# Optimization experiments

Measured on AMD Instinct MI355X. Metric: run time of the kernel, lower is better.

Reference implementation:

```python
import jax, jax.numpy as jnp
import numpy as np

N_HEAD = 4
D_MODEL = 256
D_K = D_MODEL // N_HEAD  # 64


def setup_inputs() -> dict:
    key = jax.random.key(0)
    ks = jax.random.split(key, 7)
    B, S = 4, 2048
    # xavier-uniform-ish scale for weights
    def xav(k, shape):
        fan_in, fan_out = shape[1], shape[0]
        lim = float(np.sqrt(6.0 / (fan_in + fan_out)))
        return jax.random.uniform(k, shape, jnp.float32, -lim, lim)
    return {
        "q": jax.random.normal(ks[0], (B, S, D_MODEL), jnp.float32),
        "k": jax.random.normal(ks[1], (B, S, D_MODEL), jnp.float32),
        "v": jax.random.normal(ks[2], (B, S, D_MODEL), jnp.float32),
        # per-head projection weights, stacked: [H, d_k, d_model]
        "Wq": jnp.stack([xav(jax.random.fold_in(ks[3], i), (D_K, D_MODEL)) for i in range(N_HEAD)]),
        "Wk": jnp.stack([xav(jax.random.fold_in(ks[4], i), (D_K, D_MODEL)) for i in range(N_HEAD)]),
        # v_layer is SHARED across heads: [d_v, d_model]
        "Wv": xav(ks[5], (D_K, D_MODEL)),
        # output projection: [d_model, d_v]
        "Wh": xav(ks[6], (D_MODEL, D_K)),
    }


def reference(q, k, v, Wq, Wk, Wv, Wh):
    # per-head projections (batched over heads)
    qs = jnp.einsum('bsd,hed->bhse', q, Wq)          # [B,H,S,d_k]
    ks_ = jnp.einsum('bsd,hed->bhse', k, Wk)         # [B,H,S,d_k]
    vs = jnp.einsum('bsd,ed->bse', v, Wv)            # shared v: [B,S,d_v]
    scale = jnp.sqrt(jnp.asarray(D_K, jnp.float32))
    scores = jnp.einsum('bhse,bhte->bhst', qs, ks_) / scale  # [B,H,S,S]
    attn = jax.nn.softmax(scores, axis=-1)
    heads = jnp.einsum('bhst,bte->bhse', attn, vs)   # [B,H,S,d_v]
    pooled = jnp.mean(heads, axis=1)                 # mean over heads: [B,S,d_v]
    out = jnp.einsum('bse,fe->bsf', pooled, Wh)      # [B,S,d_model]
    # original stacks attns at dim=2 -> [B,S,H,S]
    attn_out = jnp.transpose(attn, (0, 2, 1, 3))
    return out, attn_out
```

## Files before the change

kernel.cpp:

```cpp
#include <hip/hip_runtime.h>
#include <hip/hip_bf16.h>
#include <math.h>

#define B 4
#define S 2048
#define H 4
#define DK 64
#define DM 256

using bf16x8 = __attribute__((ext_vector_type(8))) short;
using bf16x4 = __attribute__((ext_vector_type(4))) short;
using f32x4 = __attribute__((ext_vector_type(4))) float;
typedef unsigned char u8;

__device__ inline ushort f2b(float f) {
  __hip_bfloat16 h = __float2bfloat16(f);
  ushort u; __builtin_memcpy(&u, &h, 2); return u;
}
__device__ inline float b2f(ushort u) {
  __hip_bfloat16 h; __builtin_memcpy(&h, &u, 2); return __bfloat162float(h);
}
__device__ inline float b2f_s(short s) { return b2f((ushort)s); }
__device__ inline bf16x8 ld8(const ushort* p) {
  return *reinterpret_cast<const bf16x8*>(p);
}
__device__ inline bf16x4 ld4(const ushort* p) {
  return *reinterpret_cast<const bf16x4*>(p);
}
#define MFMA(a, b, c) __builtin_amdgcn_mfma_f32_16x16x32_bf16((a), (b), (c), 0, 0, 0)

#if __has_builtin(__builtin_amdgcn_mfma_f32_16x16x16bf16_1k)
__device__ inline f32x4 MFMA16(bf16x4 a, bf16x4 b, f32x4 c) {
  return __builtin_amdgcn_mfma_f32_16x16x16bf16_1k(a, b, c, 0, 0, 0);
}
#else
__device__ inline f32x4 MFMA16(bf16x4 a, bf16x4 b, f32x4 c) {
  asm("v_mfma_f32_16x16x16_bf16 %0, %1, %2, %0" : "+v"(c) : "v"(a), "v"(b));
  return c;
}
#endif

__global__ __launch_bounds__(256) void wsplit_kernel(
    const float* __restrict__ Wq, const float* __restrict__ Wk,
    const float* __restrict__ Wv, const float* __restrict__ Wh,
    ushort* __restrict__ wqh, ushort* __restrict__ wql,
    ushort* __restrict__ wkh, ushort* __restrict__ wkl,
    ushort* __restrict__ wvh, ushort* __restrict__ wvl,
    ushort* __restrict__ whh, ushort* __restrict__ whl) {
  const int row = blockIdx.x;
  const int t = threadIdx.x;
  if (row < 576) {
    const float* src; ushort* dh; ushort* dl; int r;
    if (row < 256) { src = Wq; dh = wqh; dl = wql; r = row; }
    else if (row < 512) { src = Wk; dh = wkh; dl = wkl; r = row - 256; }
    else { src = Wv; dh = wvh; dl = wvl; r = row - 512; }
    const float v = src[(size_t)r * DM + t];
    const ushort hi = f2b(v);
    dh[(size_t)r * DM + t] = hi;
    dl[(size_t)r * DM + t] = f2b(v - b2f(hi));
  } else if (t < 64) {
    const int r = row - 576;
    const float v = Wh[(size_t)r * DK + t];
    const ushort hi = f2b(v);
    whh[(size_t)r * DK + t] = hi;
    whl[(size_t)r * DK + t] = f2b(v - b2f(hi));
  }
}

__global__ __launch_bounds__(256) void proj_qk2(
    const float* __restrict__ q, const float* __restrict__ k,
    const ushort* __restrict__ wqh, const ushort* __restrict__ wql,
    const ushort* __restrict__ wkh, const ushort* __restrict__ wkl,
    ushort* __restrict__ qhi, ushort* __restrict__ qlo,
    ushort* __restrict__ khi, ushort* __restrict__ klo) {
  const int which = blockIdx.x >> 9;
  const int sub = blockIdx.x & 511;
  const int tile = sub & 127;
  const int h = sub >> 7;
  const float* x = which ? k : q;
  const ushort* wh = which ? wkh : wqh;
  const ushort* wl = which ? wkl : wql;
  ushort* ohi = which ? khi : qhi;
  ushort* olo = which ? klo : qlo;

  const int wid = threadIdx.x >> 6;
  const int lane = threadIdx.x & 63;
  const int l15 = lane & 15, g = lane >> 4;
  const int row0 = tile * 64 + wid * 16;

  bf16x8 ah[8], al[8];
  const float* xrow = x + (size_t)(row0 + l15) * DM;
#pragma unroll
  for (int ks = 0; ks < 8; ++ks) {
    float4 f0 = *(const float4*)(xrow + ks * 32 + 8 * g);
    float4 f1 = *(const float4*)(xrow + ks * 32 + 8 * g + 4);
    float fv[8] = {f0.x, f0.y, f0.z, f0.w, f1.x, f1.y, f1.z, f1.w};
    bf16x8 h8, l8;
#pragma unroll
    for (int j = 0; j < 8; ++j) {
      ushort hu = f2b(fv[j]);
      h8[j] = (short)hu;
      l8[j] = (short)f2b(fv[j] - b2f(hu));
    }
    ah[ks] = h8; al[ks] = l8;
  }

  f32x4 acc[4];
#pragma unroll
  for (int n = 0; n < 4; ++n) acc[n] = (f32x4){0.f, 0.f, 0.f, 0.f};

#pragma unroll
  for (int n = 0; n < 4; ++n) {
    const ushort* wrh = wh + (size_t)(h * DK + n * 16 + l15) * DM + 8 * g;
    const ushort* wrl = wl + (size_t)(h * DK + n * 16 + l15) * DM + 8 * g;
#pragma unroll
    for (int ks = 0; ks < 8; ++ks) {
      bf16x8 bh = ld8(wrh + ks * 32);
      bf16x8 bl = ld8(wrl + ks * 32);
      acc[n] = MFMA(ah[ks], bh, acc[n]);
      acc[n] = MFMA(al[ks], bh, acc[n]);
      acc[n] = MFMA(ah[ks], bl, acc[n]);
    }
  }

#pragma unroll
  for (int n = 0; n < 4; ++n) {
    const int e = n * 16 + l15;
#pragma unroll
    for (int r = 0; r < 4; ++r) {
      const int tok = row0 + 4 * g + r;
      const int b = tok >> 11, s = tok & (S - 1);
      const size_t idx = ((size_t)((b * H + h) * S + s)) * DK + e;
      const float val = acc[n][r];
      const ushort hu = f2b(val);
      ohi[idx] = hu;
      olo[idx] = f2b(val - b2f(hu));
    }
  }
}

__global__ __launch_bounds__(256) void proj_v(
    const float* __restrict__ x, const ushort* __restrict__ wh,
    const ushort* __restrict__ wl, ushort* __restrict__ vT) {
  const int wid = threadIdx.x >> 6;
  const int lane = threadIdx.x & 63;
  const int l15 = lane & 15, g = lane >> 4;
  const int row0 = blockIdx.x * 64 + wid * 16;

  bf16x8 ah[8], al[8];
  const float* xrow = x + (size_t)(row0 + l15) * DM;
#pragma unroll
  for (int ks = 0; ks < 8; ++ks) {
    float4 f0 = *(const float4*)(xrow + ks * 32 + 8 * g);
    float4 f1 = *(const float4*)(xrow + ks * 32 + 8 * g + 4);
    float fv[8] = {f0.x, f0.y, f0.z, f0.w, f1.x, f1.y, f1.z, f1.w};
    bf16x8 h8, l8;
#pragma unroll
    for (int j = 0; j < 8; ++j) {
      ushort hu = f2b(fv[j]);
      h8[j] = (short)hu;
      l8[j] = (short)f2b(fv[j] - b2f(hu));
    }
    ah[ks] = h8; al[ks] = l8;
  }

  f32x4 acc[4];
#pragma unroll
  for (int n = 0; n < 4; ++n) acc[n] = (f32x4){0.f, 0.f, 0.f, 0.f};
#pragma unroll
  for (int n = 0; n < 4; ++n) {
    const ushort* wrh = wh + (size_t)(n * 16 + l15) * DM + 8 * g;
    const ushort* wrl = wl + (size_t)(n * 16 + l15) * DM + 8 * g;
#pragma unroll
    for (int ks = 0; ks < 8; ++ks) {
      bf16x8 bh = ld8(wrh + ks * 32);
      bf16x8 bl = ld8(wrl + ks * 32);
      acc[n] = MFMA(ah[ks], bh, acc[n]);
      acc[n] = MFMA(al[ks], bh, acc[n]);
      acc[n] = MFMA(ah[ks], bl, acc[n]);
    }
  }
#pragma unroll
  for (int n = 0; n < 4; ++n) {
    const int e = n * 16 + l15;
#pragma unroll
    for (int r = 0; r < 4; ++r) {
      const int tok = row0 + 4 * g + r;
      const int b = tok >> 11, s = tok & (S - 1);
      vT[((size_t)b * DK + e) * S + s] = f2b(acc[n][r]);
    }
  }
}

__global__ __launch_bounds__(512) void attn_kernel(
    const ushort* __restrict__ qhi, const ushort* __restrict__ qlo,
    const ushort* __restrict__ khi, const ushort* __restrict__ klo,
    const ushort* __restrict__ vT,
    float* __restrict__ attn_out, float* __restrict__ heads) {
  __shared__ __align__(16) u8 kst[2][8192];
  __shared__ __align__(16) u8 vst[2][5120];

  const int tid = threadIdx.x;
  const int wid = tid >> 6;
  const int lane = tid & 63;
  const int l15 = lane & 15, g = lane >> 4;
  const int bid = blockIdx.x;
  const int swz = (bid & 7) * 32 + (bid >> 3);
  const int qt = swz & 15;
  const int h = (swz >> 4) & 3;
  const int b = swz >> 6;
  const int row0 = qt * 128 + wid * 16;
  const float SC = 0.125f;

  const size_t bh = (size_t)(b * H + h);
  const ushort* qbh = qhi + (bh * S + row0 + l15) * DK;
  const ushort* qbl = qlo + (bh * S + row0 + l15) * DK;
  const bf16x8 aqh0 = ld8(qbh + 8 * g), aqh1 = ld8(qbh + 32 + 8 * g);
  const bf16x8 aql0 = ld8(qbl + 8 * g), aql1 = ld8(qbl + 32 + 8 * g);
  const ushort* kbh = khi + bh * S * DK;
  const ushort* kbl = klo + bh * S * DK;
  const ushort* vTb = vT + (size_t)b * DK * S;

  const int role = tid >> 8;
  const int t8 = tid & 255;
  const int skey = t8 >> 3, sslot = t8 & 7;
  const int sgslot = sslot ^ (skey & 7);
  const ushort* ksrc = role ? kbl : kbh;
  const int kdst = role * 4096 + t8 * 16;
  const int sdim = tid >> 3, sk8 = tid & 7;

  const int fx0 = l15 * 128 + ((g ^ (l15 & 7)) << 4);
  const int fx1 = l15 * 128 + (((4 + g) ^ (l15 & 7)) << 4);
  const int fy0 = fx0 + 2048;
  const int fy1 = fx1 + 2048;

  float ssum = 0.f;
  if (role == 0)
    *(bf16x8*)(&kst[0][t8 * 16]) = ld8(kbh + (size_t)skey * DK + sgslot * 8);
  __syncthreads();
  for (int c = 0; c < 64; ++c) {
    const int p = c & 1;
    bf16x8 rkh;
    if (c + 1 < 64 && role == 0)
      rkh = ld8(kbh + (size_t)((c + 1) * 32 + skey) * DK + sgslot * 8);
    const u8* kb = kst[p];
    bf16x8 bh0 = *(const bf16x8*)(kb + fx0);
    bf16x8 bh1 = *(const bf16x8*)(kb + fx1);
    bf16x8 ch0 = *(const bf16x8*)(kb + fy0);
    bf16x8 ch1 = *(const bf16x8*)(kb + fy1);
    f32x4 a0 = {0.f, 0.f, 0.f, 0.f}, a1 = {0.f, 0.f, 0.f, 0.f};
    a0 = MFMA(bh0, aqh0, a0); a0 = MFMA(bh1, aqh1, a0);
    a1 = MFMA(ch0, aqh0, a1); a1 = MFMA(ch1, aqh1, a1);
    ssum += ((__expf(a0[0] * SC) + __expf(a0[1] * SC)) +
             (__expf(a0[2] * SC) + __expf(a0[3] * SC))) +
            ((__expf(a1[0] * SC) + __expf(a1[1] * SC)) +
             (__expf(a1[2] * SC) + __expf(a1[3] * SC)));
    if (c + 1 < 64 && role == 0) *(bf16x8*)(&kst[p ^ 1][t8 * 16]) = rkh;
    __syncthreads();
  }
  ssum += __shfl_xor(ssum, 16, 64);
  ssum += __shfl_xor(ssum, 32, 64);
  const float inv = 1.f / ssum;

  f32x4 hacc[4] = {{0.f, 0.f, 0.f, 0.f}, {0.f, 0.f, 0.f, 0.f},
                   {0.f, 0.f, 0.f, 0.f}, {0.f, 0.f, 0.f, 0.f}};
  float* arow = attn_out + (((size_t)(b * S + row0 + l15)) * H + h) * S;

  *(bf16x8*)(&kst[0][kdst]) = ld8(ksrc + (size_t)skey * DK + sgslot * 8);
  *(bf16x4*)(&vst[0][sdim * 80 + sk8 * 8]) = ld4(vTb + (size_t)sdim * S + sk8 * 4);
  __syncthreads();

  for (int c = 0; c < 64; ++c) {
    const int p = c & 1;
    const int t0 = c * 32;
    bf16x8 rk; bf16x4 rv;
    if (c + 1 < 64) {
      const size_t t1 = (size_t)(c + 1) * 32;
      rk = ld8(ksrc + (t1 + skey) * DK + sgslot * 8);
      rv = ld4(vTb + (size_t)sdim * S + t1 + sk8 * 4);
    }
    const u8* kb = kst[p];
    const u8* vb = vst[p];
    bf16x8 bh0 = *(const bf16x8*)(kb + fx0);
    bf16x8 bh1 = *(const bf16x8*)(kb + fx1);
    bf16x8 ch0 = *(const bf16x8*)(kb + fy0);
    bf16x8 ch1 = *(const bf16x8*)(kb + fy1);
    bf16x8 bl0 = *(const bf16x8*)(kb + 4096 + fx0);
    bf16x8 bl1 = *(const bf16x8*)(kb + 4096 + fx1);
    bf16x8 cl0 = *(const bf16x8*)(kb + 4096 + fy0);
    bf16x8 cl1 = *(const bf16x8*)(kb + 4096 + fy1);
    f32x4 a0 = {0.f, 0.f, 0.f, 0.f}, a1 = {0.f, 0.f, 0.f, 0.f};
    a0 = MFMA(bh0, aqh0, a0); a0 = MFMA(bh1, aqh1, a0);
    a0 = MFMA(bl0, aqh0, a0); a0 = MFMA(bl1, aqh1, a0);
    a0 = MFMA(bh0, aql0, a0); a0 = MFMA(bh1, aql1, a0);
    a1 = MFMA(ch0, aqh0, a1); a1 = MFMA(ch1, aqh1, a1);
    a1 = MFMA(cl0, aqh0, a1); a1 = MFMA(cl1, aqh1, a1);
    a1 = MFMA(ch0, aql0, a1); a1 = MFMA(ch1, aql1, a1);

    const float p0 = __expf(a0[0] * SC) * inv;
    const float p1 = __expf(a0[1] * SC) * inv;
    const float p2 = __expf(a0[2] * SC) * inv;
    const float p3 = __expf(a0[3] * SC) * inv;
    const float p4 = __expf(a1[0] * SC) * inv;
    const float p5 = __expf(a1[1] * SC) * inv;
    const float p6 = __expf(a1[2] * SC) * inv;
    const float p7 = __expf(a1[3] * SC) * inv;

    f32x4 o0 = {p0, p1, p2, p3};
    f32x4 o1 = {p4, p5, p6, p7};
    __builtin_nontemporal_store(o0, (f32x4*)(arow + t0 + 4 * g));
    __builtin_nontemporal_store(o1, (f32x4*)(arow + t0 + 16 + 4 * g));

    bf16x4 pa0, pa1;
    pa0[0] = (short)f2b(p0); pa0[1] = (short)f2b(p1);
    pa0[2] = (short)f2b(p2); pa0[3] = (short)f2b(p3);
    pa1[0] = (short)f2b(p4); pa1[1] = (short)f2b(p5);
    pa1[2] = (short)f2b(p6); pa1[3] = (short)f2b(p7);

#pragma unroll
    for (int n = 0; n < 4; ++n) {
      bf16x4 vb0 = *(const bf16x4*)(vb + (n * 16 + l15) * 80 + 8 * g);
      bf16x4 vb1 = *(const bf16x4*)(vb + (n * 16 + l15) * 80 + 32 + 8 * g);
      hacc[n] = MFMA16(pa0, vb0, hacc[n]);
      hacc[n] = MFMA16(pa1, vb1, hacc[n]);
    }

    if (c + 1 < 64) {
      *(bf16x8*)(&kst[p ^ 1][kdst]) = rk;
      *(bf16x4*)(&vst[p ^ 1][sdim * 80 + sk8 * 8]) = rv;
    }
    __syncthreads();
  }

#pragma unroll
  for (int n = 0; n < 4; ++n)
#pragma unroll
    for (int r = 0; r < 4; ++r)
      heads[(bh * S + row0 + 4 * g + r) * DK + n * 16 + l15] = hacc[n][r];
}

__global__ __launch_bounds__(256) void out_mfma(
    const float* __restrict__ heads, const ushort* __restrict__ whh,
    const ushort* __restrict__ whl, float* __restrict__ out) {
  const int wid = threadIdx.x >> 6;
  const int lane = threadIdx.x & 63;
  const int l15 = lane & 15, g = lane >> 4;
  const int row0 = blockIdx.x * 16;
  const int tok = row0 + l15;
  const int b = tok >> 11, s = tok & (S - 1);

  bf16x8 ah[2], al[2];
  const float* hp0 = heads + ((size_t)((b * H + 0) * S + s)) * DK;
  const size_t hstride = (size_t)S * DK;
#pragma unroll
  for (int c = 0; c < 2; ++c) {
    const int d0 = c * 32 + 8 * g;
    float4 s0 = {0.f, 0.f, 0.f, 0.f}, s1 = {0.f, 0.f, 0.f, 0.f};
#pragma unroll
    for (int hh = 0; hh < H; ++hh) {
      const float* hp = hp0 + hh * hstride + d0;
      float4 x0 = *(const float4*)hp;
      float4 x1 = *(const float4*)(hp + 4);
      s0.x += x0.x; s0.y += x0.y; s0.z += x0.z; s0.w += x0.w;
      s1.x += x1.x; s1.y += x1.y; s1.z += x1.z; s1.w += x1.w;
    }
    float fv[8] = {s0.x * 0.25f, s0.y * 0.25f, s0.z * 0.25f, s0.w * 0.25f,
                   s1.x * 0.25f, s1.y * 0.25f, s1.z * 0.25f, s1.w * 0.25f};
    bf16x8 h8, l8;
#pragma unroll
    for (int j = 0; j < 8; ++j) {
      ushort hu = f2b(fv[j]);
      h8[j] = (short)hu;
      l8[j] = (short)f2b(fv[j] - b2f(hu));
    }
    ah[c] = h8; al[c] = l8;
  }

  f32x4 acc[4];
#pragma unroll
  for (int n = 0; n < 4; ++n) acc[n] = (f32x4){0.f, 0.f, 0.f, 0.f};
#pragma unroll
  for (int n = 0; n < 4; ++n) {
    const int f = wid * 64 + n * 16 + l15;
    const ushort* brh = whh + (size_t)f * DK + 8 * g;
    const ushort* brl = whl + (size_t)f * DK + 8 * g;
#pragma unroll
    for (int c = 0; c < 2; ++c) {
      bf16x8 bh = ld8(brh + c * 32);
      bf16x8 bl = ld8(brl + c * 32);
      acc[n] = MFMA(ah[c], bh, acc[n]);
      acc[n] = MFMA(al[c], bh, acc[n]);
      acc[n] = MFMA(ah[c], bl, acc[n]);
    }
  }

#pragma unroll
  for (int n = 0; n < 4; ++n) {
    const int f = wid * 64 + n * 16 + l15;
#pragma unroll
    for (int r = 0; r < 4; ++r)
      out[(size_t)(row0 + 4 * g + r) * DM + f] = acc[n][r];
  }
}

extern "C" void kernel_launch(void* const* d_in, const int* in_sizes, int n_in,
                              void* d_out, int out_size, void* d_ws, size_t ws_size,
                              hipStream_t stream) {
  const float* q = (const float*)d_in[0];
  const float* k = (const float*)d_in[1];
  const float* v = (const float*)d_in[2];
  const float* Wq = (const float*)d_in[3];
  const float* Wk = (const float*)d_in[4];
  const float* Wv = (const float*)d_in[5];
  const float* Wh = (const float*)d_in[6];

  float* out = (float*)d_out;
  float* attn_out = out + (size_t)B * S * DM;

  const size_t n1 = (size_t)B * H * S * DK;
  ushort* qhi = (ushort*)d_ws;
  ushort* qlo = qhi + n1;
  ushort* khi = qlo + n1;
  ushort* klo = khi + n1;
  ushort* vT = klo + n1;
  float* heads = (float*)(vT + (size_t)B * DK * S);
  ushort* wqh = (ushort*)(heads + n1);
  ushort* wql = wqh + (size_t)H * DK * DM;
  ushort* wkh = wql + (size_t)H * DK * DM;
  ushort* wkl = wkh + (size_t)H * DK * DM;
  ushort* wvh = wkl + (size_t)H * DK * DM;
  ushort* wvl = wvh + (size_t)DK * DM;
  ushort* whh = wvl + (size_t)DK * DM;
  ushort* whl = whh + (size_t)DM * DK;

  wsplit_kernel<<<832, 256, 0, stream>>>(Wq, Wk, Wv, Wh, wqh, wql, wkh, wkl,
                                         wvh, wvl, whh, whl);
  proj_qk2<<<1024, 256, 0, stream>>>(q, k, wqh, wql, wkh, wkl, qhi, qlo, khi, klo);
  proj_v<<<128, 256, 0, stream>>>(v, wvh, wvl, vT);
  attn_kernel<<<256, 512, 0, stream>>>(qhi, qlo, khi, klo, vT, attn_out, heads);
  out_mfma<<<512, 256, 0, stream>>>(heads, whh, whl, out);
}
```

Baseline: 170.4 us.

## Merge Q/K/V projections into one launch and enlarge attention key tiles

The V projection is folded into the Q/K projection kernel as extra blocks, which removes one kernel launch and lets V share the same wave. In the attention kernel the key chunk grows from 32 to 128 keys in the row-sum pass and to 64 keys in the output pass, with all 512 threads now loading K hi and lo. This cuts the number of loop iterations and barriers. MFMA sections are wrapped in s_setprio, at the cost of doubled LDS use, which may reduce occupancy.

New measurement: 183.1 us. +7.4%, slower.

```diff
diff --git a/kernel.cpp b/kernel.cpp
--- a/kernel.cpp
+++ b/kernel.cpp
@@ -20,12 +20,8 @@
 __device__ inline float b2f(ushort u) {
   __hip_bfloat16 h; __builtin_memcpy(&h, &u, 2); return __bfloat162float(h);
 }
-__device__ inline float b2f_s(short s) { return b2f((ushort)s); }
 __device__ inline bf16x8 ld8(const ushort* p) {
   return *reinterpret_cast<const bf16x8*>(p);
-}
-__device__ inline bf16x4 ld4(const ushort* p) {
-  return *reinterpret_cast<const bf16x4*>(p);
 }
 #define MFMA(a, b, c) __builtin_amdgcn_mfma_f32_16x16x32_bf16((a), (b), (c), 0, 0, 0)
 
@@ -67,26 +63,35 @@
   }
 }
 
-__global__ __launch_bounds__(256) void proj_qk2(
+__global__ __launch_bounds__(256) void proj_all(
     const float* __restrict__ q, const float* __restrict__ k,
+    const float* __restrict__ v,
     const ushort* __restrict__ wqh, const ushort* __restrict__ wql,
     const ushort* __restrict__ wkh, const ushort* __restrict__ wkl,
+    const ushort* __restrict__ wvh, const ushort* __restrict__ wvl,
     ushort* __restrict__ qhi, ushort* __restrict__ qlo,
-    ushort* __restrict__ khi, ushort* __restrict__ klo) {
-  const int which = blockIdx.x >> 9;
-  const int sub = blockIdx.x & 511;
-  const int tile = sub & 127;
-  const int h = sub >> 7;
-  const float* x = which ? k : q;
-  const ushort* wh = which ? wkh : wqh;
-  const ushort* wl = which ? wkl : wql;
-  ushort* ohi = which ? khi : qhi;
-  ushort* olo = which ? klo : qlo;
-
+    ushort* __restrict__ khi, ushort* __restrict__ klo,
+    ushort* __restrict__ vT) {
+  const int bid = blockIdx.x;
   const int wid = threadIdx.x >> 6;
   const int lane = threadIdx.x & 63;
   const int l15 = lane & 15, g = lane >> 4;
-  const int row0 = tile * 64 + wid * 16;
+
+  const float* x; const ushort* wh; const ushort* wl;
+  int row0, h;
+  if (bid < 1024) {
+    const int which = bid >> 9;
+    const int sub = bid & 511;
+    const int tile = sub & 127;
+    h = sub >> 7;
+    x = which ? k : q;
+    wh = which ? wkh : wqh;
+    wl = which ? wkl : wql;
+    row0 = tile * 64 + wid * 16;
+  } else {
+    x = v; wh = wvh; wl = wvl; h = 0;
+    row0 = (bid - 1024) * 64 + wid * 16;
+  }
 
   bf16x8 ah[8], al[8];
   const float* xrow = x + (size_t)(row0 + l15) * DM;
@@ -108,7 +113,6 @@
   f32x4 acc[4];
 #pragma unroll
   for (int n = 0; n < 4; ++n) acc[n] = (f32x4){0.f, 0.f, 0.f, 0.f};
-
 #pragma unroll
   for (int n = 0; n < 4; ++n) {
     const ushort* wrh = wh + (size_t)(h * DK + n * 16 + l15) * DM + 8 * g;
@@ -123,71 +127,33 @@
     }
   }
 
-#pragma unroll
-  for (int n = 0; n < 4; ++n) {
-    const int e = n * 16 + l15;
-#pragma unroll
-    for (int r = 0; r < 4; ++r) {
-      const int tok = row0 + 4 * g + r;
-      const int b = tok >> 11, s = tok & (S - 1);
-      const size_t idx = ((size_t)((b * H + h) * S + s)) * DK + e;
-      const float val = acc[n][r];
-      const ushort hu = f2b(val);
-      ohi[idx] = hu;
-      olo[idx] = f2b(val - b2f(hu));
-    }
-  }
-}
-
-__global__ __launch_bounds__(256) void proj_v(
-    const float* __restrict__ x, const ushort* __restrict__ wh,
-    const ushort* __restrict__ wl, ushort* __restrict__ vT) {
-  const int wid = threadIdx.x >> 6;
-  const int lane = threadIdx.x & 63;
-  const int l15 = lane & 15, g = lane >> 4;
-  const int row0 = blockIdx.x * 64 + wid * 16;
-
-  bf16x8 ah[8], al[8];
-  const float* xrow = x + (size_t)(row0 + l15) * DM;
-#pragma unroll
-  for (int ks = 0; ks < 8; ++ks) {
-    float4 f0 = *(const float4*)(xrow + ks * 32 + 8 * g);
-    float4 f1 = *(const float4*)(xrow + ks * 32 + 8 * g + 4);
-    float fv[8] = {f0.x, f0.y, f0.z, f0.w, f1.x, f1.y, f1.z, f1.w};
-    bf16x8 h8, l8;
-#pragma unroll
-    for (int j = 0; j < 8; ++j) {
-      ushort hu = f2b(fv[j]);
-      h8[j] = (short)hu;
-      l8[j] = (short)f2b(fv[j] - b2f(hu));
-    }
-    ah[ks] = h8; al[ks] = l8;
-  }
-
-  f32x4 acc[4];
-#pragma unroll
-  for (int n = 0; n < 4; ++n) acc[n] = (f32x4){0.f, 0.f, 0.f, 0.f};
-#pragma unroll
-  for (int n = 0; n < 4; ++n) {
-    const ushort* wrh = wh + (size_t)(n * 16 + l15) * DM + 8 * g;
-    const ushort* wrl = wl + (size_t)(n * 16 + l15) * DM + 8 * g;
-#pragma unroll
-    for (int ks = 0; ks < 8; ++ks) {
-      bf16x8 bh = ld8(wrh + ks * 32);
-      bf16x8 bl = ld8(wrl + ks * 32);
-      acc[n] = MFMA(ah[ks], bh, acc[n]);
-      acc[n] = MFMA(al[ks], bh, acc[n]);
-      acc[n] = MFMA(ah[ks], bl, acc[n]);
-    }
-  }
-#pragma unroll
-  for (int n = 0; n < 4; ++n) {
-    const int e = n * 16 + l15;
-#pragma unroll
-    for (int r = 0; r < 4; ++r) {
-      const int tok = row0 + 4 * g + r;
-      const int b = tok >> 11, s = tok & (S - 1);
-      vT[((size_t)b * DK + e) * S + s] = f2b(acc[n][r]);
+  if (bid < 1024) {
+    ushort* ohi = (bid >> 9) ? khi : qhi;
+    ushort* olo = (bid >> 9) ? klo : qlo;
+#pragma unroll
+    for (int n = 0; n < 4; ++n) {
+      const int e = n * 16 + l15;
+#pragma unroll
+      for (int r = 0; r < 4; ++r) {
+        const int tok = row0 + 4 * g + r;
+        const int b = tok >> 11, s = tok & (S - 1);
+        const size_t idx = ((size_t)((b * H + h) * S + s)) * DK + e;
+        const float val = acc[n][r];
+        const ushort hu = f2b(val);
+        ohi[idx] = hu;
+        olo[idx] = f2b(val - b2f(hu));
+      }
+    }
+  } else {
+#pragma unroll
+    for (int n = 0; n < 4; ++n) {
+      const int e = n * 16 + l15;
+#pragma unroll
+      for (int r = 0; r < 4; ++r) {
+        const int tok = row0 + 4 * g + r;
+        const int b = tok >> 11, s = tok & (S - 1);
+        vT[((size_t)b * DK + e) * S + s] = f2b(acc[n][r]);
+      }
     }
   }
 }
@@ -197,8 +163,8 @@
     const ushort* __restrict__ khi, const ushort* __restrict__ klo,
     const ushort* __restrict__ vT,
     float* __restrict__ attn_out, float* __restrict__ heads) {
-  __shared__ __align__(16) u8 kst[2][8192];
-  __shared__ __align__(16) u8 vst[2][5120];
+  __shared__ __align__(16) u8 kst[2][16384];
+  __shared__ __align__(16) u8 vst[2][10240];
 
   const int tid = threadIdx.x;
   const int wid = tid >> 6;
@@ -221,42 +187,45 @@
   const ushort* kbl = klo + bh * S * DK;
   const ushort* vTb = vT + (size_t)b * DK * S;
 
-  const int role = tid >> 8;
-  const int t8 = tid & 255;
-  const int skey = t8 >> 3, sslot = t8 & 7;
+  const int skey = tid >> 3, sslot = tid & 7;
   const int sgslot = sslot ^ (skey & 7);
-  const ushort* ksrc = role ? kbl : kbh;
-  const int kdst = role * 4096 + t8 * 16;
   const int sdim = tid >> 3, sk8 = tid & 7;
 
   const int fx0 = l15 * 128 + ((g ^ (l15 & 7)) << 4);
   const int fx1 = l15 * 128 + (((4 + g) ^ (l15 & 7)) << 4);
-  const int fy0 = fx0 + 2048;
-  const int fy1 = fx1 + 2048;
 
   float ssum = 0.f;
-  if (role == 0)
-    *(bf16x8*)(&kst[0][t8 * 16]) = ld8(kbh + (size_t)skey * DK + sgslot * 8);
-  __syncthreads();
-  for (int c = 0; c < 64; ++c) {
-    const int p = c & 1;
-    bf16x8 rkh;
-    if (c + 1 < 64 && role == 0)
-      rkh = ld8(kbh + (size_t)((c + 1) * 32 + skey) * DK + sgslot * 8);
-    const u8* kb = kst[p];
-    bf16x8 bh0 = *(const bf16x8*)(kb + fx0);
-    bf16x8 bh1 = *(const bf16x8*)(kb + fx1);
-    bf16x8 ch0 = *(const bf16x8*)(kb + fy0);
-    bf16x8 ch1 = *(const bf16x8*)(kb + fy1);
-    f32x4 a0 = {0.f, 0.f, 0.f, 0.f}, a1 = {0.f, 0.f, 0.f, 0.f};
-    a0 = MFMA(bh0, aqh0, a0); a0 = MFMA(bh1, aqh1, a0);
-    a1 = MFMA(ch0, aqh0, a1); a1 = MFMA(ch1, aqh1, a1);
-    ssum += ((__expf(a0[0] * SC) + __expf(a0[1] * SC)) +
-             (__expf(a0[2] * SC) + __expf(a0[3] * SC))) +
-            ((__expf(a1[0] * SC) + __expf(a1[1] * SC)) +
-             (__expf(a1[2] * SC) + __expf(a1[3] * SC)));
-    if (c + 1 < 64 && role == 0) *(bf16x8*)(&kst[p ^ 1][t8 * 16]) = rkh;
+  {
+    *(bf16x8*)(&kst[0][tid * 16]) = ld8(kbh + (size_t)skey * DK + sgslot * 8);
+    *(bf16x8*)(&kst[0][8192 + tid * 16]) =
+        ld8(kbh + (size_t)(skey + 64) * DK + sgslot * 8);
     __syncthreads();
+    for (int c = 0; c < 16; ++c) {
+      const int p = c & 1;
+      bf16x8 r0, r1;
+      if (c + 1 < 16) {
+        const size_t t1 = (size_t)(c + 1) * 128;
+        r0 = ld8(kbh + (t1 + skey) * DK + sgslot * 8);
+        r1 = ld8(kbh + (t1 + skey + 64) * DK + sgslot * 8);
+      }
+      const u8* kb = kst[p];
+      __builtin_amdgcn_s_setprio(1);
+#pragma unroll
+      for (int kg = 0; kg < 8; ++kg) {
+        bf16x8 bh0 = *(const bf16x8*)(kb + kg * 2048 + fx0);
+        bf16x8 bh1 = *(const bf16x8*)(kb + kg * 2048 + fx1);
+        f32x4 a = {0.f, 0.f, 0.f, 0.f};
+        a = MFMA(bh0, aqh0, a); a = MFMA(bh1, aqh1, a);
+        ssum += (__expf(a[0] * SC) + __expf(a[1] * SC)) +
+                (__expf(a[2] * SC) + __expf(a[3] * SC));
+      }
+      __builtin_amdgcn_s_setprio(0);
+      if (c + 1 < 16) {
+        *(bf16x8*)(&kst[p ^ 1][tid * 16]) = r0;
+        *(bf16x8*)(&kst[p ^ 1][8192 + tid * 16]) = r1;
+      }
+      __syncthreads();
+    }
   }
   ssum += __shfl_xor(ssum, 16, 64);
   ssum += __shfl_xor(ssum, 32, 64);
@@ -266,68 +235,57 @@
                    {0.f, 0.f, 0.f, 0.f}, {0.f, 0.f, 0.f, 0.f}};
   float* arow = attn_out + (((size_t)(b * S + row0 + l15)) * H + h) * S;
 
-  *(bf16x8*)(&kst[0][kdst]) = ld8(ksrc + (size_t)skey * DK + sgslot * 8);
-  *(bf16x4*)(&vst[0][sdim * 80 + sk8 * 8]) = ld4(vTb + (size_t)sdim * S + sk8 * 4);
+  *(bf16x8*)(&kst[0][tid * 16]) = ld8(kbh + (size_t)skey * DK + sgslot * 8);
+  *(bf16x8*)(&kst[0][8192 + tid * 16]) = ld8(kbl + (size_t)skey * DK + sgslot * 8);
+  *(bf16x8*)(&vst[0][sdim * 160 + sk8 * 16]) = ld8(vTb + (size_t)sdim * S + sk8 * 8);
   __syncthreads();
 
-  for (int c = 0; c < 64; ++c) {
+  for (int c = 0; c < 32; ++c) {
     const int p = c & 1;
-    const int t0 = c * 32;
-    bf16x8 rk; bf16x4 rv;
-    if (c + 1 < 64) {
-      const size_t t1 = (size_t)(c + 1) * 32;
-      rk = ld8(ksrc + (t1 + skey) * DK + sgslot * 8);
-      rv = ld4(vTb + (size_t)sdim * S + t1 + sk8 * 4);
+    const int t0 = c * 64;
+    bf16x8 rh, rl, rv;
+    if (c + 1 < 32) {
+      const size_t t1 = (size_t)(c + 1) * 64;
+      rh = ld8(kbh + (t1 + skey) * DK + sgslot * 8);
+      rl = ld8(kbl + (t1 + skey) * DK + sgslot * 8);
+      rv = ld8(vTb + (size_t)sdim * S + t1 + sk8 * 8);
     }
     const u8* kb = kst[p];
     const u8* vb = vst[p];
-    bf16x8 bh0 = *(const bf16x8*)(kb + fx0);
-    bf16x8 bh1 = *(const bf16x8*)(kb + fx1);
-    bf16x8 ch0 = *(const bf16x8*)(kb + fy0);
-    bf16x8 ch1 = *(const bf16x8*)(kb + fy1);
-    bf16x8 bl0 = *(const bf16x8*)(kb + 4096 + fx0);
-    bf16x8 bl1 = *(const bf16x8*)(kb + 4096 + fx1);
-    bf16x8 cl0 = *(const bf16x8*)(kb + 4096 + fy0);
-    bf16x8 cl1 = *(const bf16x8*)(kb + 4096 + fy1);
-    f32x4 a0 = {0.f, 0.f, 0.f, 0.f}, a1 = {0.f, 0.f, 0.f, 0.f};
-    a0 = MFMA(bh0, aqh0, a0); a0 = MFMA(bh1, aqh1, a0);
-    a0 = MFMA(bl0, aqh0, a0); a0 = MFMA(bl1, aqh1, a0);
-    a0 = MFMA(bh0, aql0, a0); a0 = MFMA(bh1, aql1, a0);
-    a1 = MFMA(ch0, aqh0, a1); a1 = MFMA(ch1, aqh1, a1);
-    a1 = MFMA(cl0, aqh0, a1); a1 = MFMA(cl1, aqh1, a1);
-    a1 = MFMA(ch0, aql0, a1); a1 = MFMA(ch1, aql1, a1);
-
-    const float p0 = __expf(a0[0] * SC) * inv;
-    const float p1 = __expf(a0[1] * SC) * inv;
-    const float p2 = __expf(a0[2] * SC) * inv;
-    const float p3 = __expf(a0[3] * SC) * inv;
-    const float p4 = __expf(a1[0] * SC) * inv;
-    const float p5 = __expf(a1[1] * SC) * inv;
-    const float p6 = __expf(a1[2] * SC) * inv;
-    const float p7 = __expf(a1[3] * SC) * inv;
-
-    f32x4 o0 = {p0, p1, p2, p3};
-    f32x4 o1 = {p4, p5, p6, p7};
-    __builtin_nontemporal_store(o0, (f32x4*)(arow + t0 + 4 * g));
-    __builtin_nontemporal_store(o1, (f32x4*)(arow + t0 + 16 + 4 * g));
-
-    bf16x4 pa0, pa1;
-    pa0[0] = (short)f2b(p0); pa0[1] = (short)f2b(p1);
-    pa0[2] = (short)f2b(p2); pa0[3] = (short)f2b(p3);
-    pa1[0] = (short)f2b(p4); pa1[1] = (short)f2b(p5);
-    pa1[2] = (short)f2b(p6); pa1[3] = (short)f2b(p7);
-
-#pragma unroll
-    for (int n = 0; n < 4; ++n) {
-      bf16x4 vb0 = *(const bf16x4*)(vb + (n * 16 + l15) * 80 + 8 * g);
-      bf16x4 vb1 = *(const bf16x4*)(vb + (n * 16 + l15) * 80 + 32 + 8 * g);
-      hacc[n] = MFMA16(pa0, vb0, hacc[n]);
-      hacc[n] = MFMA16(pa1, vb1, hacc[n]);
-    }
-
-    if (c + 1 < 64) {
-      *(bf16x8*)(&kst[p ^ 1][kdst]) = rk;
-      *(bf16x4*)(&vst[p ^ 1][sdim * 80 + sk8 * 8]) = rv;
+    __builtin_amdgcn_s_setprio(1);
+#pragma unroll
+    for (int kg = 0; kg < 4; ++kg) {
+      bf16x8 bh0 = *(const bf16x8*)(kb + kg * 2048 + fx0);
+      bf16x8 bh1 = *(const bf16x8*)(kb + kg * 2048 + fx1);
+      bf16x8 bl0 = *(const bf16x8*)(kb + 8192 + kg * 2048 + fx0);
+      bf16x8 bl1 = *(const bf16x8*)(kb + 8192 + kg * 2048 + fx1);
+      f32x4 a = {0.f, 0.f, 0.f, 0.f};
+      a = MFMA(bh0, aqh0, a); a = MFMA(bh1, aqh1, a);
+      a = MFMA(bl0, aqh0, a); a = MFMA(bl1, aqh1, a);
+      a = MFMA(bh0, aql0, a); a = MFMA(bh1, aql1, a);
+
+      const float p0 = __expf(a[0] * SC) * inv;
+      const float p1 = __expf(a[1] * SC) * inv;
+      const float p2 = __expf(a[2] * SC) * inv;
+      const float p3 = __expf(a[3] * SC) * inv;
+
+      f32x4 o = {p0, p1, p2, p3};
+      __builtin_nontemporal_store(o, (f32x4*)(arow + t0 + kg * 16 + 4 * g));
+
+      bf16x4 pa;
+      pa[0] = (short)f2b(p0); pa[1] = (short)f2b(p1);
+      pa[2] = (short)f2b(p2); pa[3] = (short)f2b(p3);
+#pragma unroll
+      for (int n = 0; n < 4; ++n) {
+        bf16x4 vb0 = *(const bf16x4*)(vb + (n * 16 + l15) * 160 + kg * 32 + 8 * g);
+        hacc[n] = MFMA16(pa, vb0, hacc[n]);
+      }
+    }
+    __builtin_amdgcn_s_setprio(0);
+    if (c + 1 < 32) {
+      *(bf16x8*)(&kst[p ^ 1][tid * 16]) = rh;
+      *(bf16x8*)(&kst[p ^ 1][8192 + tid * 16]) = rl;
+      *(bf16x8*)(&vst[p ^ 1][sdim * 160 + sk8 * 16]) = rv;
     }
     __syncthreads();
   }
@@ -435,8 +393,8 @@
 
   wsplit_kernel<<<832, 256, 0, stream>>>(Wq, Wk, Wv, Wh, wqh, wql, wkh, wkl,
                                          wvh, wvl, whh, whl);
-  proj_qk2<<<1024, 256, 0, stream>>>(q, k, wqh, wql, wkh, wkl, qhi, qlo, khi, klo);
-  proj_v<<<128, 256, 0, stream>>>(v, wvh, wvl, vT);
+  proj_all<<<1152, 256, 0, stream>>>(q, k, v, wqh, wql, wkh, wkl, wvh, wvl,
+                                     qhi, qlo, khi, klo, vT);
   attn_kernel<<<256, 512, 0, stream>>>(qhi, qlo, khi, klo, vT, attn_out, heads);
   out_mfma<<<512, 256, 0, stream>>>(heads, whh, whl, out);
 }
```
